# Optimization experiments

Hardware: AMD Instinct MI355X
Metric: run time of the kernel (lower is better)

The kernel has to match this reference:

```python
import jax, jax.numpy as jnp
from jax import lax
import numpy as np

B, H, W, C = 32, 384, 384, 8
FIELD = 7
NUM_ITERS = 5


def setup_inputs() -> dict:
    key = jax.random.key(0)
    k1, k2, k3 = jax.random.split(key, 3)
    x = jax.random.normal(k1, (B, H, W, C), dtype=jnp.float32)
    # k_internal: [field, field, C_in, C_out]; original init is zeros, use small
    # random values so the mean-field iterations are non-trivial.
    k_internal = jax.random.normal(k2, (FIELD, FIELD, C, C), dtype=jnp.float32) * 0.02
    # 1x1 conv (k_scale) weight + bias
    k_scale_w = jax.random.normal(k3, (C, C), dtype=jnp.float32) * (1.0 / np.sqrt(C))
    k_scale_b = jnp.zeros((C,), dtype=jnp.float32)
    return {"x": x, "k_internal": k_internal, "k_scale_w": k_scale_w,
            "k_scale_b": k_scale_b, "num_iters": NUM_ITERS}


def reference(x, k_internal, k_scale_w, k_scale_b, num_iters):
    C_ = x.shape[-1]
    # off-diagonal channel-pair mask, broadcast over spatial kernel dims
    mask = (1.0 - jnp.eye(C_, dtype=x.dtype))[None, None]  # [1,1,C,C]
    k = k_internal * mask
    q = jax.nn.softmax(x, axis=-1)                 # [B,H,W,C]
    u = -jnp.log(jnp.clip(q, 1e-6, 1.0))           # unary potentials
    logits = x
    for _ in range(num_iters):
        penalty = lax.conv_general_dilated(
            q, k, window_strides=(1, 1), padding='SAME',
            dimension_numbers=('NHWC', 'HWIO', 'NHWC'))
        logits = -(u + penalty)
        logits = jnp.einsum('bhwc,cd->bhwd', logits, k_scale_w) + k_scale_b
        q = jax.nn.softmax(logits, axis=-1)
    return logits
```

## Files before the change

### kernel.cpp

```cpp
#include <hip/hip_runtime.h>
#include <math.h>

#define Cc     8
#define FIELD  7
#define PAD    3
#define TW     32
#define TH     16
#define HAW    38
#define HAH    22
#define QSTR   39
#define NSTG   (HAH*QSTR)
#define BB     32
#define HH     384
#define WW     384
#define NB     4
#define NSLOT  64
#define UCLIP  13.815510557964274f

typedef __attribute__((ext_vector_type(8))) short short8;
typedef __attribute__((ext_vector_type(4))) float f32x4;

__device__ __forceinline__ unsigned short f2bf(float f) {
    unsigned u = __float_as_uint(f);
    u += 0x7FFFu + ((u >> 16) & 1u);
    return (unsigned short)(u >> 16);
}
__device__ __forceinline__ unsigned short f2h(float f) {
    return __builtin_bit_cast(unsigned short, (_Float16)f);
}
__device__ __forceinline__ float hlo(unsigned u) {
    return (float)__builtin_bit_cast(_Float16, (unsigned short)(u & 0xFFFFu));
}
__device__ __forceinline__ float hhi(unsigned u) {
    return (float)__builtin_bit_cast(_Float16, (unsigned short)(u >> 16));
}

__global__ __launch_bounds__(256)
void prep_w(const float* __restrict__ kw, const float* __restrict__ sw,
            unsigned short* __restrict__ wtab) {
    int it = blockIdx.x * 256 + threadIdx.x;
    if (it >= NSLOT * 8) return;
    int s = it >> 3, j = it & 7;
    int dyp = s >> 3, dx = s & 7;
#pragma unroll
    for (int n = 0; n < 16; ++n) {
        int h = n >> 3, d = n & 7;
        int dy = dyp - h;
        float a = 0.f;
        if (dy >= 0 && dy < FIELD && dx < 7) {
            int tap = dy * 7 + dx;
#pragma unroll
            for (int c = 0; c < Cc; ++c) {
                float kv = (c == j) ? 0.f : kw[(tap * Cc + j) * Cc + c];
                a = fmaf(kv, sw[c * Cc + d], a);
            }
        }
        wtab[(s * 16 + n) * 8 + j] = f2bf(a);
    }
}

__global__ __launch_bounds__(256)
void init_qv(const float* __restrict__ x, const float* __restrict__ sw,
             const float* __restrict__ sb,
             uint4* __restrict__ q0, float* __restrict__ vf,
             uint4* __restrict__ vh, int half) {
    long long p = (long long)blockIdx.x * 256 + threadIdx.x;
    const float4* xp = (const float4*)(x + p * Cc);
    float4 a0 = xp[0], a1 = xp[1];
    float xv[Cc] = {a0.x, a0.y, a0.z, a0.w, a1.x, a1.y, a1.z, a1.w};
    float m = xv[0];
#pragma unroll
    for (int c = 1; c < Cc; ++c) m = fmaxf(m, xv[c]);
    float s = 0.f, e[Cc];
#pragma unroll
    for (int c = 0; c < Cc; ++c) { e[c] = __expf(xv[c] - m); s += e[c]; }
    float inv = 1.f / s;
    uint4 qo;
    qo.x = f2bf(e[0] * inv) | ((unsigned)f2bf(e[1] * inv) << 16);
    qo.y = f2bf(e[2] * inv) | ((unsigned)f2bf(e[3] * inv) << 16);
    qo.z = f2bf(e[4] * inv) | ((unsigned)f2bf(e[5] * inv) << 16);
    qo.w = f2bf(e[6] * inv) | ((unsigned)f2bf(e[7] * inv) << 16);
    q0[p] = qo;

    float lse = m + __logf(s);
    float u[Cc];
#pragma unroll
    for (int c = 0; c < Cc; ++c) u[c] = fminf(lse - xv[c], UCLIP);
    float vv[Cc];
#pragma unroll
    for (int d = 0; d < Cc; ++d) {
        float a = sb[d];
#pragma unroll
        for (int c = 0; c < Cc; ++c) a = fmaf(-u[c], sw[c * Cc + d], a);
        vv[d] = a;
    }
    if (half) {
        uint4 vo;
        vo.x = f2h(vv[0]) | ((unsigned)f2h(vv[1]) << 16);
        vo.y = f2h(vv[2]) | ((unsigned)f2h(vv[3]) << 16);
        vo.z = f2h(vv[4]) | ((unsigned)f2h(vv[5]) << 16);
        vo.w = f2h(vv[6]) | ((unsigned)f2h(vv[7]) << 16);
        vh[p] = vo;
    } else {
        float4* vp = (float4*)(vf + p * Cc);
        vp[0] = make_float4(vv[0], vv[1], vv[2], vv[3]);
        vp[1] = make_float4(vv[4], vv[5], vv[6], vv[7]);
    }
}

template<int VHALF>
__global__ __launch_bounds__(512)
void mrf_iter(const uint4* __restrict__ qin,
              const unsigned short* __restrict__ wtab,
              const void* __restrict__ vsrc,
              uint4* __restrict__ qout,
              float* __restrict__ lout,
              int last) {
    __shared__ __align__(16) uint4 qs[2][NSTG];

    const int tid = threadIdx.x;
    const int wv  = tid >> 6;
    const int l   = tid & 63;
    const int m   = l & 15;
    const int g   = l >> 4;

    const int w0 = blockIdx.x * TW;
    const int h0 = blockIdx.y * TH;
    const int b0 = blockIdx.z * NB;

    const int r0 = 4 * (wv >> 1);
    const int cx = 16 * (wv & 1);

    const int p   = g & 1;
    const int row = r0 + 2 * p + (g >> 1);
    const int px  = cx + m;
    const long long pixoff = (long long)(h0 + row) * WW + (w0 + px);
    const long long BSTR   = (long long)HH * WW;

    short8 bw[8][2];
#pragma unroll
    for (int dyq = 0; dyq < 8; ++dyq)
#pragma unroll
        for (int dxb = 0; dxb < 2; ++dxb) {
            int s = dyq * 8 + 4 * dxb + g;
            uint4 t = *(const uint4*)(wtab + (s * 16 + m) * 8);
            bw[dyq][dxb] = __builtin_bit_cast(short8, t);
        }

    const int sy0 = tid / QSTR, sx0 = tid - sy0 * QSTR;
    const int gh0 = h0 + sy0 - PAD, gw0 = w0 + sx0 - PAD;
    const bool in0 = (gh0 >= 0 && gh0 < HH && gw0 >= 0 && gw0 < WW);
    const long long off0 = (long long)gh0 * WW + gw0;
    const int  s1  = tid + 512;
    const bool has1 = (s1 < NSTG);
    const int sy1 = s1 / QSTR, sx1 = s1 - sy1 * QSTR;
    const int gh1 = h0 + sy1 - PAD, gw1 = w0 + sx1 - PAD;
    const bool in1 = has1 && (gh1 >= 0 && gh1 < HH && gw1 >= 0 && gw1 < WW);
    const long long off1 = (long long)gh1 * WW + gw1;

    const uint4* qb = qin + b0 * BSTR;
    const uint4  zz = make_uint4(0, 0, 0, 0);

    uint4 c0 = in0 ? qb[off0] : zz;
    uint4 c1 = in1 ? qb[off1] : zz;
    uint4  vhv = zz;
    float4 v0, v1;
    if constexpr (VHALF) {
        vhv = ((const uint4*)vsrc)[b0 * BSTR + pixoff];
    } else {
        const float4* vp0 = (const float4*)((const float*)vsrc + (b0 * BSTR + pixoff) * Cc);
        v0 = vp0[0]; v1 = vp0[1];
    }
    qs[0][tid] = c0;
    if (has1) qs[0][s1] = c1;
    __syncthreads();

#pragma unroll
    for (int t = 0; t < NB; ++t) {
        uint4 n0 = zz, n1 = zz, vhn = zz;
        float4 vn0 = make_float4(0.f, 0.f, 0.f, 0.f), vn1 = vn0;
        if (t + 1 < NB) {
            const uint4* qbn = qb + (t + 1) * BSTR;
            n0 = in0 ? qbn[off0] : zz;
            n1 = in1 ? qbn[off1] : zz;
            if constexpr (VHALF) {
                vhn = ((const uint4*)vsrc)[(b0 + t + 1) * BSTR + pixoff];
            } else {
                const float4* vpn = (const float4*)((const float*)vsrc + ((b0 + t + 1) * BSTR + pixoff) * Cc);
                vn0 = vpn[0]; vn1 = vpn[1];
            }
        }

        f32x4 acc0 = (f32x4){0.f, 0.f, 0.f, 0.f};
        f32x4 acc1 = (f32x4){0.f, 0.f, 0.f, 0.f};
        const uint4* Q = qs[t & 1];
        const int colbase = cx + m + g;
#pragma unroll
        for (int dyp = 0; dyp < 10; ++dyp) {
            const int rb = (r0 + dyp) * QSTR + colbase;
#pragma unroll
            for (int dxb = 0; dxb < 2; ++dxb) {
                short8 qv = *(const short8*)&Q[rb + 4 * dxb];
                if (dyp < 8)
                    acc0 = __builtin_amdgcn_mfma_f32_16x16x32_bf16(bw[dyp][dxb], qv, acc0, 0, 0, 0);
                if (dyp >= 2)
                    acc1 = __builtin_amdgcn_mfma_f32_16x16x32_bf16(bw[dyp - 2][dxb], qv, acc1, 0, 0, 0);
            }
        }

        float o[Cc];
#pragma unroll
        for (int tt = 0; tt < 4; ++tt) {
            float s0v = __shfl_xor(acc0[tt], 16);
            float s1v = __shfl_xor(acc1[tt], 16);
            o[tt]     = p ? s1v      : acc0[tt];
            o[4 + tt] = p ? acc1[tt] : s0v;
        }

        float vv[Cc];
        if constexpr (VHALF) {
            vv[0] = hlo(vhv.x); vv[1] = hhi(vhv.x);
            vv[2] = hlo(vhv.y); vv[3] = hhi(vhv.y);
            vv[4] = hlo(vhv.z); vv[5] = hhi(vhv.z);
            vv[6] = hlo(vhv.w); vv[7] = hhi(vhv.w);
        } else {
            vv[0] = v0.x; vv[1] = v0.y; vv[2] = v0.z; vv[3] = v0.w;
            vv[4] = v1.x; vv[5] = v1.y; vv[6] = v1.z; vv[7] = v1.w;
        }
#pragma unroll
        for (int d = 0; d < Cc; ++d) o[d] = vv[d] - o[d];
        const long long pix = (b0 + t) * BSTR + pixoff;
        if (last) {
            float4* op = (float4*)(lout + pix * Cc);
            op[0] = make_float4(o[0], o[1], o[2], o[3]);
            op[1] = make_float4(o[4], o[5], o[6], o[7]);
        } else {
            float mm = o[0];
#pragma unroll
            for (int d = 1; d < Cc; ++d) mm = fmaxf(mm, o[d]);
            float ss = 0.f, e[Cc];
#pragma unroll
            for (int d = 0; d < Cc; ++d) { e[d] = __expf(o[d] - mm); ss += e[d]; }
            float inv = 1.f / ss;
            uint4 qo;
            qo.x = f2bf(e[0] * inv) | ((unsigned)f2bf(e[1] * inv) << 16);
            qo.y = f2bf(e[2] * inv) | ((unsigned)f2bf(e[3] * inv) << 16);
            qo.z = f2bf(e[4] * inv) | ((unsigned)f2bf(e[5] * inv) << 16);
            qo.w = f2bf(e[6] * inv) | ((unsigned)f2bf(e[7] * inv) << 16);
            qout[pix] = qo;
        }

        if (t + 1 < NB) {
            qs[(t + 1) & 1][tid] = n0;
            if (has1) qs[(t + 1) & 1][s1] = n1;
            __syncthreads();
            if constexpr (VHALF) { vhv = vhn; } else { v0 = vn0; v1 = vn1; }
        }
    }
}

extern "C" void kernel_launch(void* const* d_in, const int* in_sizes, int n_in,
                              void* d_out, int out_size, void* d_ws, size_t ws_size,
                              hipStream_t stream) {
    (void)in_sizes; (void)n_in; (void)out_size;
    const float* x  = (const float*)d_in[0];
    const float* kw = (const float*)d_in[1];
    const float* sw = (const float*)d_in[2];
    const float* sb = (const float*)d_in[3];

    const size_t QSZ = (size_t)BB * HH * WW * 16;
    const size_t VSZ = (size_t)BB * HH * WW * 16;
    uint4* qA = (uint4*)d_ws;
    uint4* qB = (uint4*)((char*)d_ws + QSZ);

    const long long npix = (long long)BB * HH * WW;
    dim3 grid(WW / TW, HH / TH, BB / NB);

    if (ws_size >= 2 * QSZ + VSZ + 16384) {
        uint4* vh = (uint4*)((char*)d_ws + 2 * QSZ);
        unsigned short* wt = (unsigned short*)((char*)d_ws + 2 * QSZ + VSZ);
        prep_w<<<2, 256, 0, stream>>>(kw, sw, wt);
        init_qv<<<(int)(npix / 256), 256, 0, stream>>>(x, sw, sb, qA, nullptr, vh, 1);
        mrf_iter<1><<<grid, 512, 0, stream>>>(qA, wt, vh, qB, nullptr, 0);
        mrf_iter<1><<<grid, 512, 0, stream>>>(qB, wt, vh, qA, nullptr, 0);
        mrf_iter<1><<<grid, 512, 0, stream>>>(qA, wt, vh, qB, nullptr, 0);
        mrf_iter<1><<<grid, 512, 0, stream>>>(qB, wt, vh, qA, nullptr, 0);
        mrf_iter<1><<<grid, 512, 0, stream>>>(qA, wt, vh, nullptr, (float*)d_out, 1);
    } else {
        float* vbuf = (float*)d_out;
        unsigned short* wt = (unsigned short*)((char*)d_ws + 2 * QSZ);
        prep_w<<<2, 256, 0, stream>>>(kw, sw, wt);
        init_qv<<<(int)(npix / 256), 256, 0, stream>>>(x, sw, sb, qA, vbuf, nullptr, 0);
        mrf_iter<0><<<grid, 512, 0, stream>>>(qA, wt, vbuf, qB, nullptr, 0);
        mrf_iter<0><<<grid, 512, 0, stream>>>(qB, wt, vbuf, qA, nullptr, 0);
        mrf_iter<0><<<grid, 512, 0, stream>>>(qA, wt, vbuf, qB, nullptr, 0);
        mrf_iter<0><<<grid, 512, 0, stream>>>(qB, wt, vbuf, qA, nullptr, 0);
        mrf_iter<0><<<grid, 512, 0, stream>>>(qA, wt, vbuf, nullptr, (float*)d_out, 1);
    }
}
```

Measured before the change: 359.1 us.

## Fuse softmax/unary init into first mean-field iteration kernel

Replaces the separate init_qv pass plus first mrf_iter with a fused mrf_first kernel. It reads x directly, computes the softmax q for the haloed tile in shared memory, and computes and stores the unary term v for interior pixels, then runs the first convolution and softmax iteration. This avoids writing q0 to global memory and reading it back, at the cost of recomputing softmax for halo pixels and extra shared memory for v.

```diff
diff --git a/kernel.cpp b/kernel.cpp
--- a/kernel.cpp
+++ b/kernel.cpp
@@ -35,6 +35,41 @@
     return (float)__builtin_bit_cast(_Float16, (unsigned short)(u >> 16));
 }
 
+__device__ __forceinline__ void px_qv(const float xv[Cc],
+                                      const float* __restrict__ sw,
+                                      const float* __restrict__ sb,
+                                      bool inter, uint4& qp, uint4& vp) {
+    float m = xv[0];
+#pragma unroll
+    for (int c = 1; c < Cc; ++c) m = fmaxf(m, xv[c]);
+    float s = 0.f, e[Cc];
+#pragma unroll
+    for (int c = 0; c < Cc; ++c) { e[c] = __expf(xv[c] - m); s += e[c]; }
+    float inv = 1.f / s;
+    qp.x = f2bf(e[0] * inv) | ((unsigned)f2bf(e[1] * inv) << 16);
+    qp.y = f2bf(e[2] * inv) | ((unsigned)f2bf(e[3] * inv) << 16);
+    qp.z = f2bf(e[4] * inv) | ((unsigned)f2bf(e[5] * inv) << 16);
+    qp.w = f2bf(e[6] * inv) | ((unsigned)f2bf(e[7] * inv) << 16);
+    if (inter) {
+        float lse = m + __logf(s);
+        float u[Cc];
+#pragma unroll
+        for (int c = 0; c < Cc; ++c) u[c] = fminf(lse - xv[c], UCLIP);
+        float vv[Cc];
+#pragma unroll
+        for (int d = 0; d < Cc; ++d) {
+            float a = sb[d];
+#pragma unroll
+            for (int c = 0; c < Cc; ++c) a = fmaf(-u[c], sw[c * Cc + d], a);
+            vv[d] = a;
+        }
+        vp.x = f2h(vv[0]) | ((unsigned)f2h(vv[1]) << 16);
+        vp.y = f2h(vv[2]) | ((unsigned)f2h(vv[3]) << 16);
+        vp.z = f2h(vv[4]) | ((unsigned)f2h(vv[5]) << 16);
+        vp.w = f2h(vv[6]) | ((unsigned)f2h(vv[7]) << 16);
+    }
+}
+
 __global__ __launch_bounds__(256)
 void prep_w(const float* __restrict__ kw, const float* __restrict__ sw,
             unsigned short* __restrict__ wtab) {
@@ -62,8 +97,7 @@
 __global__ __launch_bounds__(256)
 void init_qv(const float* __restrict__ x, const float* __restrict__ sw,
              const float* __restrict__ sb,
-             uint4* __restrict__ q0, float* __restrict__ vf,
-             uint4* __restrict__ vh, int half) {
+             uint4* __restrict__ q0, float* __restrict__ vf) {
     long long p = (long long)blockIdx.x * 256 + threadIdx.x;
     const float4* xp = (const float4*)(x + p * Cc);
     float4 a0 = xp[0], a1 = xp[1];
@@ -94,17 +128,166 @@
         for (int c = 0; c < Cc; ++c) a = fmaf(-u[c], sw[c * Cc + d], a);
         vv[d] = a;
     }
-    if (half) {
-        uint4 vo;
-        vo.x = f2h(vv[0]) | ((unsigned)f2h(vv[1]) << 16);
-        vo.y = f2h(vv[2]) | ((unsigned)f2h(vv[3]) << 16);
-        vo.z = f2h(vv[4]) | ((unsigned)f2h(vv[5]) << 16);
-        vo.w = f2h(vv[6]) | ((unsigned)f2h(vv[7]) << 16);
-        vh[p] = vo;
-    } else {
-        float4* vp = (float4*)(vf + p * Cc);
-        vp[0] = make_float4(vv[0], vv[1], vv[2], vv[3]);
-        vp[1] = make_float4(vv[4], vv[5], vv[6], vv[7]);
+    float4* vp = (float4*)(vf + p * Cc);
+    vp[0] = make_float4(vv[0], vv[1], vv[2], vv[3]);
+    vp[1] = make_float4(vv[4], vv[5], vv[6], vv[7]);
+}
+
+__global__ __launch_bounds__(512)
+void mrf_first(const float* __restrict__ x,
+               const unsigned short* __restrict__ wtab,
+               const float* __restrict__ sw, const float* __restrict__ sb,
+               uint4* __restrict__ vh,
+               uint4* __restrict__ qout) {
+    __shared__ __align__(16) uint4 qs[2][NSTG];
+    __shared__ __align__(16) uint4 vs[2][TH * TW];
+
+    const int tid = threadIdx.x;
+    const int wv  = tid >> 6;
+    const int l   = tid & 63;
+    const int m   = l & 15;
+    const int g   = l >> 4;
+
+    const int w0 = blockIdx.x * TW;
+    const int h0 = blockIdx.y * TH;
+    const int b0 = blockIdx.z * NB;
+
+    const int r0 = 4 * (wv >> 1);
+    const int cx = 16 * (wv & 1);
+
+    const int p   = g & 1;
+    const int row = r0 + 2 * p + (g >> 1);
+    const int px  = cx + m;
+    const long long pixoff = (long long)(h0 + row) * WW + (w0 + px);
+    const long long BSTR   = (long long)HH * WW;
+
+    short8 bw[8][2];
+#pragma unroll
+    for (int dyq = 0; dyq < 8; ++dyq)
+#pragma unroll
+        for (int dxb = 0; dxb < 2; ++dxb) {
+            int s = dyq * 8 + 4 * dxb + g;
+            uint4 t = *(const uint4*)(wtab + (s * 16 + m) * 8);
+            bw[dyq][dxb] = __builtin_bit_cast(short8, t);
+        }
+
+    const int sy0 = tid / QSTR, sx0 = tid - sy0 * QSTR;
+    const int gh0 = h0 + sy0 - PAD, gw0 = w0 + sx0 - PAD;
+    const bool in0 = (gh0 >= 0 && gh0 < HH && gw0 >= 0 && gw0 < WW);
+    const bool it0 = (sy0 >= PAD && sy0 < PAD + TH && sx0 >= PAD && sx0 < PAD + TW);
+    const int  vi0 = (sy0 - PAD) * TW + (sx0 - PAD);
+    const long long off0 = (long long)gh0 * WW + gw0;
+    const int  s1  = tid + 512;
+    const bool has1 = (s1 < NSTG);
+    const int sy1 = s1 / QSTR, sx1 = s1 - sy1 * QSTR;
+    const int gh1 = h0 + sy1 - PAD, gw1 = w0 + sx1 - PAD;
+    const bool in1 = has1 && (gh1 >= 0 && gh1 < HH && gw1 >= 0 && gw1 < WW);
+    const bool it1 = has1 && (sy1 >= PAD && sy1 < PAD + TH && sx1 >= PAD && sx1 < PAD + TW);
+    const int  vi1 = (sy1 - PAD) * TW + (sx1 - PAD);
+    const long long off1 = (long long)gh1 * WW + gw1;
+
+    const float4* xb = (const float4*)x;
+    const uint4   zz = make_uint4(0, 0, 0, 0);
+
+    {
+        float xa[Cc] = {0,0,0,0,0,0,0,0};
+        if (in0) {
+            float4 t0 = xb[(b0 * BSTR + off0) * 2], t1 = xb[(b0 * BSTR + off0) * 2 + 1];
+            xa[0]=t0.x; xa[1]=t0.y; xa[2]=t0.z; xa[3]=t0.w;
+            xa[4]=t1.x; xa[5]=t1.y; xa[6]=t1.z; xa[7]=t1.w;
+        }
+        uint4 qp = zz, vp = zz;
+        if (in0) px_qv(xa, sw, sb, it0, qp, vp);
+        qs[0][tid] = qp;
+        if (it0) { vh[b0 * BSTR + off0] = vp; vs[0][vi0] = vp; }
+        if (has1) {
+            float xc[Cc] = {0,0,0,0,0,0,0,0};
+            if (in1) {
+                float4 t0 = xb[(b0 * BSTR + off1) * 2], t1 = xb[(b0 * BSTR + off1) * 2 + 1];
+                xc[0]=t0.x; xc[1]=t0.y; xc[2]=t0.z; xc[3]=t0.w;
+                xc[4]=t1.x; xc[5]=t1.y; xc[6]=t1.z; xc[7]=t1.w;
+            }
+            uint4 qp1 = zz, vp1 = zz;
+            if (in1) px_qv(xc, sw, sb, it1, qp1, vp1);
+            qs[0][s1] = qp1;
+            if (it1) { vh[b0 * BSTR + off1] = vp1; vs[0][vi1] = vp1; }
+        }
+    }
+    __syncthreads();
+
+#pragma unroll
+    for (int t = 0; t < NB; ++t) {
+        float4 n0a = make_float4(0,0,0,0), n0b = n0a, n1a = n0a, n1b = n0a;
+        if (t + 1 < NB) {
+            const long long bo = (long long)(b0 + t + 1) * BSTR;
+            if (in0) { n0a = xb[(bo + off0) * 2]; n0b = xb[(bo + off0) * 2 + 1]; }
+            if (in1) { n1a = xb[(bo + off1) * 2]; n1b = xb[(bo + off1) * 2 + 1]; }
+        }
+
+        f32x4 acc0 = (f32x4){0.f, 0.f, 0.f, 0.f};
+        f32x4 acc1 = (f32x4){0.f, 0.f, 0.f, 0.f};
+        const uint4* Q = qs[t & 1];
+        const int colbase = cx + m + g;
+#pragma unroll
+        for (int dyp = 0; dyp < 10; ++dyp) {
+            const int rb = (r0 + dyp) * QSTR + colbase;
+#pragma unroll
+            for (int dxb = 0; dxb < 2; ++dxb) {
+                short8 qv = *(const short8*)&Q[rb + 4 * dxb];
+                if (dyp < 8)
+                    acc0 = __builtin_amdgcn_mfma_f32_16x16x32_bf16(bw[dyp][dxb], qv, acc0, 0, 0, 0);
+                if (dyp >= 2)
+                    acc1 = __builtin_amdgcn_mfma_f32_16x16x32_bf16(bw[dyp - 2][dxb], qv, acc1, 0, 0, 0);
+            }
+        }
+
+        float o[Cc];
+#pragma unroll
+        for (int tt = 0; tt < 4; ++tt) {
+            float s0v = __shfl_xor(acc0[tt], 16);
+            float s1v = __shfl_xor(acc1[tt], 16);
+            o[tt]     = p ? s1v      : acc0[tt];
+            o[4 + tt] = p ? acc1[tt] : s0v;
+        }
+
+        {
+            uint4 vhv = vs[t & 1][row * TW + px];
+            float vv[Cc] = {hlo(vhv.x), hhi(vhv.x), hlo(vhv.y), hhi(vhv.y),
+                            hlo(vhv.z), hhi(vhv.z), hlo(vhv.w), hhi(vhv.w)};
+#pragma unroll
+            for (int d = 0; d < Cc; ++d) o[d] = vv[d] - o[d];
+            float mm = o[0];
+#pragma unroll
+            for (int d = 1; d < Cc; ++d) mm = fmaxf(mm, o[d]);
+            float ss = 0.f, e[Cc];
+#pragma unroll
+            for (int d = 0; d < Cc; ++d) { e[d] = __expf(o[d] - mm); ss += e[d]; }
+            float inv = 1.f / ss;
+            uint4 qo;
+            qo.x = f2bf(e[0] * inv) | ((unsigned)f2bf(e[1] * inv) << 16);
+            qo.y = f2bf(e[2] * inv) | ((unsigned)f2bf(e[3] * inv) << 16);
+            qo.z = f2bf(e[4] * inv) | ((unsigned)f2bf(e[5] * inv) << 16);
+            qo.w = f2bf(e[6] * inv) | ((unsigned)f2bf(e[7] * inv) << 16);
+            qout[(b0 + t) * BSTR + pixoff] = qo;
+        }
+
+        if (t + 1 < NB) {
+            const int nb = (t + 1) & 1;
+            const long long bo = (long long)(b0 + t + 1) * BSTR;
+            float xa[Cc] = {n0a.x, n0a.y, n0a.z, n0a.w, n0b.x, n0b.y, n0b.z, n0b.w};
+            uint4 qp = zz, vp = zz;
+            if (in0) px_qv(xa, sw, sb, it0, qp, vp);
+            qs[nb][tid] = qp;
+            if (it0) { vh[bo + off0] = vp; vs[nb][vi0] = vp; }
+            if (has1) {
+                float xc[Cc] = {n1a.x, n1a.y, n1a.z, n1a.w, n1b.x, n1b.y, n1b.z, n1b.w};
+                uint4 qp1 = zz, vp1 = zz;
+                if (in1) px_qv(xc, sw, sb, it1, qp1, vp1);
+                qs[nb][s1] = qp1;
+                if (it1) { vh[bo + off1] = vp1; vs[nb][vi1] = vp1; }
+            }
+            __syncthreads();
+        }
     }
 }
 
@@ -280,8 +463,7 @@
         uint4* vh = (uint4*)((char*)d_ws + 2 * QSZ);
         unsigned short* wt = (unsigned short*)((char*)d_ws + 2 * QSZ + VSZ);
         prep_w<<<2, 256, 0, stream>>>(kw, sw, wt);
-        init_qv<<<(int)(npix / 256), 256, 0, stream>>>(x, sw, sb, qA, nullptr, vh, 1);
-        mrf_iter<1><<<grid, 512, 0, stream>>>(qA, wt, vh, qB, nullptr, 0);
+        mrf_first<<<grid, 512, 0, stream>>>(x, wt, sw, sb, vh, qB);
         mrf_iter<1><<<grid, 512, 0, stream>>>(qB, wt, vh, qA, nullptr, 0);
         mrf_iter<1><<<grid, 512, 0, stream>>>(qA, wt, vh, qB, nullptr, 0);
         mrf_iter<1><<<grid, 512, 0, stream>>>(qB, wt, vh, qA, nullptr, 0);
@@ -290,7 +472,7 @@
         float* vbuf = (float*)d_out;
         unsigned short* wt = (unsigned short*)((char*)d_ws + 2 * QSZ);
         prep_w<<<2, 256, 0, stream>>>(kw, sw, wt);
-        init_qv<<<(int)(npix / 256), 256, 0, stream>>>(x, sw, sb, qA, vbuf, nullptr, 0);
+        init_qv<<<(int)(npix / 256), 256, 0, stream>>>(x, sw, sb, qA, vbuf);
         mrf_iter<0><<<grid, 512, 0, stream>>>(qA, wt, vbuf, qB, nullptr, 0);
         mrf_iter<0><<<grid, 512, 0, stream>>>(qB, wt, vbuf, qA, nullptr, 0);
         mrf_iter<0><<<grid, 512, 0, stream>>>(qA, wt, vbuf, qB, nullptr, 0);
```

Result: slower. 387.7 us (+8.0%).
